# Optimization experiments

Hardware: AMD Instinct MI355X
Metric: run time of the kernel (lower is better)

Reference implementation:

```python
import jax, jax.numpy as jnp
import numpy as np

N_KNOTS = 16
DEGREE = 3
EPS = 1e-8


def make_knots(n_knots, degree):
    knots = np.zeros(n_knots, dtype=np.float32)
    for i in range(n_knots):
        if i <= degree:
            knots[i] = 0.0
        elif i >= n_knots - degree - 1:
            knots[i] = 1.0
        else:
            knots[i] = (i - degree) / (n_knots - 2 * degree - 1)
    return knots


def setup_inputs() -> dict:
    key = jax.random.key(0)
    k1, k2 = jax.random.split(key)
    x = jax.random.uniform(k1, (65536, 64), dtype=jnp.float32)
    control_points = jax.random.normal(k2, (64, 12, 64), dtype=jnp.float32)
    return {"x": x, "control_points": control_points}


def bspline_basis(x, knots_np, degree):
    # x: [B, D] in [0,1]; returns basis: [B, D, n_control_points]
    n_knots = knots_np.shape[0]
    n_intervals = n_knots - 1
    knots = jnp.asarray(knots_np)
    xe = x[..., None]  # [B, D, 1]
    left = knots[:-1]
    right = knots[1:]
    in_interval = (xe >= left) & (xe < right)
    last = (xe >= left[-1]) & (xe <= right[-1])  # include right endpoint of last interval
    basis = jnp.concatenate([in_interval[..., :-1], last], axis=-1).astype(x.dtype)
    for k in range(1, degree + 1):
        nb = n_intervals - k
        j = np.arange(nb)
        dL = knots_np[j + k] - knots_np[j]          # constants
        dR = knots_np[j + k + 1] - knots_np[j + 1]
        okL = np.abs(dL) > EPS
        okR = np.abs(dR) > EPS
        invL = jnp.asarray(np.where(okL, 1.0 / np.where(okL, dL, 1.0), 0.0).astype(np.float32))
        invR = jnp.asarray(np.where(okR, 1.0 / np.where(okR, dR, 1.0), 0.0).astype(np.float32))
        cL = (xe - knots[j]) * invL                 # [B, D, nb], zero where degenerate
        cR = (knots[j + k + 1] - xe) * invR
        basis = cL * basis[..., :nb] + cR * basis[..., 1:nb + 1]
    return basis


def reference(x, control_points):
    # x: [B, in_dim]; control_points: [in_dim, n_cp, out_dim]
    knots_np = make_knots(N_KNOTS, DEGREE)
    xc = jnp.clip(x, 0.0, 1.0)
    basis = bspline_basis(xc, knots_np, DEGREE)     # [B, in_dim, n_cp]
    return jnp.einsum('bic,ico->bo', basis, control_points)
```

## Files before the change

kernel.cpp:

```cpp
#include <hip/hip_runtime.h>


typedef short short8 __attribute__((ext_vector_type(8)));
typedef float f32x4 __attribute__((ext_vector_type(4)));
typedef unsigned u32x4 __attribute__((ext_vector_type(4)));

#define THREADS 256

static __device__ __forceinline__ unsigned bf16rne(float f) {
  unsigned u = __float_as_uint(f);
  return (u + 0x7FFFu + ((u >> 16) & 1u)) >> 16;
}

__global__ __launch_bounds__(256) void prep_wfrag(const float* __restrict__ cp,
                                                  unsigned* __restrict__ wfrag) {
  int id = blockIdx.x * 256 + threadIdx.x;
  int d  = id & 3;
  int l  = (id >> 2) & 63;
  int id2 = id >> 8;
  int nt = id2 / 24;
  int s  = id2 - nt * 24;
  int g  = l >> 4;
  int o  = nt * 16 + (l & 15);
  int k0 = 192 * g + 8 * s + 2 * d;
  unsigned lo = bf16rne(cp[k0 * 64 + o]);
  unsigned hi = bf16rne(cp[(k0 + 1) * 64 + o]);
  wfrag[id] = lo | (hi << 16);
}

struct Pack6 { unsigned w0, w1, w2, w3, w4, w5; };

static __device__ __forceinline__ Pack6 eval_pack(float xi) {
  xi = fminf(fmaxf(xi, 0.0f), 1.0f);
  float t9 = xi * 9.0f;
  int jj = (int)t9;
  float validf = (jj <= 8) ? 1.0f : 0.0f;
  jj = (jj > 8) ? 8 : jj;
  float fj = (float)jj;
  float u  = t9 - fj;
  float omu = 1.0f - u;
  float c1  = fminf(fj, 1.0f);
  float c2  = fminf(fj, 2.0f);
  float rdj = 9.0f - fj;
  float d2p = fminf(rdj, 2.0f);
  float d3p = fminf(rdj, 3.0f);
  float invA = (jj == 0) ? 1.0f : 0.5f;
  float invB = (jj == 8) ? 1.0f : 0.5f;
  float invC = (jj == 0) ? 1.0f : ((jj == 1) ? 0.5f : (1.0f / 3.0f));
  float invD = (jj == 0 || jj == 8) ? 0.5f : (1.0f / 3.0f);
  float invE = (jj >= 7) ? ((jj == 8) ? 1.0f : 0.5f) : (1.0f / 3.0f);
  float xkm1 = u + c1, xkm2 = u + c2;
  float k2x = d2p - u, k3x = d3p - u;
  float t0 = omu * invA;
  float A0 = omu * t0;
  float s1 = xkm1 * t0;
  float t1 = u * invB;
  float A1 = fmaf(k2x, t1, s1);
  float A2 = u * t1;
  float u0 = A0 * invC;
  float B0 = omu * u0;
  float s2 = xkm2 * u0;
  float u1 = A1 * invD;
  float B1 = fmaf(k2x, u1, s2);
  float s3 = xkm1 * u1;
  float u2 = A2 * invE;
  float B2 = fmaf(k3x, u2, s3);
  float B3 = u * u2;
  B0 *= validf; B1 *= validf; B2 *= validf; B3 *= validf;

  unsigned b0 = bf16rne(B0), b1 = bf16rne(B1), b2 = bf16rne(B2), b3 = bf16rne(B3);
  unsigned p01 = b0 | (b1 << 16);
  unsigned p23 = b2 | (b3 << 16);
  unsigned O0 = p01 << 16;
  unsigned O1 = (p01 >> 16) | (p23 << 16);
  unsigned O2 = p23 >> 16;
  int e2 = jj >> 1;
  bool odd = (jj & 1) != 0;
#define VE(q) ((q == e2) ? p01 : ((q == e2 + 1) ? p23 : 0u))
#define VO(q) ((q == e2) ? O0 : ((q == e2 + 1) ? O1 : ((q == e2 + 2) ? O2 : 0u)))
  Pack6 r;
  r.w0 = odd ? VO(0) : VE(0);
  r.w1 = odd ? VO(1) : VE(1);
  r.w2 = odd ? VO(2) : VE(2);
  r.w3 = odd ? VO(3) : VE(3);
  r.w4 = odd ? VO(4) : VE(4);
  r.w5 = odd ? VO(5) : VE(5);
#undef VE
#undef VO
  return r;
}

__global__ __launch_bounds__(THREADS, 4) void kan_mfma(const float* __restrict__ x,
                                                       const unsigned* __restrict__ wfrag,
                                                       float* __restrict__ out) {
  const int tid  = threadIdx.x;
  const int lane = tid & 63;
  const int w    = tid >> 6;
  const int m = lane & 15, g = lane >> 4;
  const long row0 = (long)blockIdx.x * 64 + (w >> 1) * 32;
  const int  ntb  = (w & 1) * 2;

  float xr0[16], xr1[16];
  {
    const float4* p0 = (const float4*)(x + (row0 + m) * 64 + g * 16);
    const float4* p1 = (const float4*)(x + (row0 + 16 + m) * 64 + g * 16);
    #pragma unroll
    for (int q = 0; q < 4; ++q) {
      float4 v = p0[q];
      xr0[4 * q] = v.x; xr0[4 * q + 1] = v.y; xr0[4 * q + 2] = v.z; xr0[4 * q + 3] = v.w;
    }
    #pragma unroll
    for (int q = 0; q < 4; ++q) {
      float4 v = p1[q];
      xr1[4 * q] = v.x; xr1[4 * q + 1] = v.y; xr1[4 * q + 2] = v.z; xr1[4 * q + 3] = v.w;
    }
  }

  f32x4 acc[2][2];
  #pragma unroll
  for (int mt = 0; mt < 2; ++mt)
    #pragma unroll
    for (int ntl = 0; ntl < 2; ++ntl)
      acc[mt][ntl] = f32x4{0.0f, 0.0f, 0.0f, 0.0f};

  const u32x4* wf4 = (const u32x4*)wfrag;

  #pragma unroll
  for (int q = 0; q < 8; ++q) {
    u32x4 bq0[3], bq1[3];
    #pragma unroll
    for (int sub = 0; sub < 3; ++sub) {
      bq0[sub] = wf4[((ntb + 0) * 24 + 3 * q + sub) * 64 + lane];
      bq1[sub] = wf4[((ntb + 1) * 24 + 3 * q + sub) * 64 + lane];
    }
    Pack6 aA = eval_pack(xr0[2 * q]);
    Pack6 aB = eval_pack(xr0[2 * q + 1]);
    Pack6 bA = eval_pack(xr1[2 * q]);
    Pack6 bB = eval_pack(xr1[2 * q + 1]);
    #pragma unroll
    for (int sub = 0; sub < 3; ++sub) {
      u32x4 qa, qb;
      if (sub == 0) {
        qa[0] = aA.w0; qa[1] = aA.w1; qa[2] = aA.w2; qa[3] = aA.w3;
        qb[0] = bA.w0; qb[1] = bA.w1; qb[2] = bA.w2; qb[3] = bA.w3;
      } else if (sub == 1) {
        qa[0] = aA.w4; qa[1] = aA.w5; qa[2] = aB.w0; qa[3] = aB.w1;
        qb[0] = bA.w4; qb[1] = bA.w5; qb[2] = bB.w0; qb[3] = bB.w1;
      } else {
        qa[0] = aB.w2; qa[1] = aB.w3; qa[2] = aB.w4; qa[3] = aB.w5;
        qb[0] = bB.w2; qb[1] = bB.w3; qb[2] = bB.w4; qb[3] = bB.w5;
      }
      short8 A0 = __builtin_bit_cast(short8, qa);
      short8 A1 = __builtin_bit_cast(short8, qb);
      short8 Bf0 = __builtin_bit_cast(short8, bq0[sub]);
      short8 Bf1 = __builtin_bit_cast(short8, bq1[sub]);
      acc[0][0] = __builtin_amdgcn_mfma_f32_16x16x32_bf16(A0, Bf0, acc[0][0], 0, 0, 0);
      acc[1][0] = __builtin_amdgcn_mfma_f32_16x16x32_bf16(A1, Bf0, acc[1][0], 0, 0, 0);
      acc[0][1] = __builtin_amdgcn_mfma_f32_16x16x32_bf16(A0, Bf1, acc[0][1], 0, 0, 0);
      acc[1][1] = __builtin_amdgcn_mfma_f32_16x16x32_bf16(A1, Bf1, acc[1][1], 0, 0, 0);
    }
  }

  #pragma unroll
  for (int mt = 0; mt < 2; ++mt)
    #pragma unroll
    for (int ntl = 0; ntl < 2; ++ntl)
      #pragma unroll
      for (int j = 0; j < 4; ++j)
        out[(row0 + mt * 16 + g * 4 + j) * 64 + (ntb + ntl) * 16 + m] = acc[mt][ntl][j];
}

extern "C" void kernel_launch(void* const* d_in, const int* in_sizes, int n_in,
                              void* d_out, int out_size, void* d_ws, size_t ws_size,
                              hipStream_t stream) {
  const float* x  = (const float*)d_in[0];
  const float* cp = (const float*)d_in[1];
  float* out = (float*)d_out;
  unsigned* wfrag = (unsigned*)d_ws;

  hipLaunchKernelGGL(prep_wfrag, dim3(96), dim3(256), 0, stream, cp, wfrag);
  const int rows = in_sizes[0] / 64;
  hipLaunchKernelGGL(kan_mfma, dim3(rows / 64), dim3(THREADS), 0, stream,
                     x, wfrag, out);
}
```

Before: 100.8 us.

## Give each wave 16 rows by all 64 outputs and pack basis via 64-bit shifts

Each wave now owns 16 rows and all four output tiles, instead of 32 rows and two output tiles. Each basis value is therefore evaluated once per wave rather than twice across paired waves, and the A fragments are built with a 64-bit shift of the packed bf16 quad instead of a chain of selects. The cost is that every wave loads twice as many weight fragments (4x3 u32x4 per step), which raises global/L2 traffic and register pressure.

```diff
diff --git a/kernel.cpp b/kernel.cpp
--- a/kernel.cpp
+++ b/kernel.cpp
@@ -4,6 +4,7 @@
 typedef short short8 __attribute__((ext_vector_type(8)));
 typedef float f32x4 __attribute__((ext_vector_type(4)));
 typedef unsigned u32x4 __attribute__((ext_vector_type(4)));
+typedef unsigned long long u64;
 
 #define THREADS 256
 
@@ -28,9 +29,7 @@
   wfrag[id] = lo | (hi << 16);
 }
 
-struct Pack6 { unsigned w0, w1, w2, w3, w4, w5; };
-
-static __device__ __forceinline__ Pack6 eval_pack(float xi) {
+static __device__ __forceinline__ void eval_chunks(float xi, u64& c0, u64& c1, u64& c2) {
   xi = fminf(fmaxf(xi, 0.0f), 1.0f);
   float t9 = xi * 9.0f;
   int jj = (int)t9;
@@ -39,8 +38,8 @@
   float fj = (float)jj;
   float u  = t9 - fj;
   float omu = 1.0f - u;
-  float c1  = fminf(fj, 1.0f);
-  float c2  = fminf(fj, 2.0f);
+  float k1c = fminf(fj, 1.0f);
+  float k2c = fminf(fj, 2.0f);
   float rdj = 9.0f - fj;
   float d2p = fminf(rdj, 2.0f);
   float d3p = fminf(rdj, 3.0f);
@@ -49,7 +48,7 @@
   float invC = (jj == 0) ? 1.0f : ((jj == 1) ? 0.5f : (1.0f / 3.0f));
   float invD = (jj == 0 || jj == 8) ? 0.5f : (1.0f / 3.0f);
   float invE = (jj >= 7) ? ((jj == 8) ? 1.0f : 0.5f) : (1.0f / 3.0f);
-  float xkm1 = u + c1, xkm2 = u + c2;
+  float xkm1 = u + k1c, xkm2 = u + k2c;
   float k2x = d2p - u, k3x = d3p - u;
   float t0 = omu * invA;
   float A0 = omu * t0;
@@ -68,26 +67,20 @@
   float B3 = u * u2;
   B0 *= validf; B1 *= validf; B2 *= validf; B3 *= validf;
 
-  unsigned b0 = bf16rne(B0), b1 = bf16rne(B1), b2 = bf16rne(B2), b3 = bf16rne(B3);
-  unsigned p01 = b0 | (b1 << 16);
-  unsigned p23 = b2 | (b3 << 16);
-  unsigned O0 = p01 << 16;
-  unsigned O1 = (p01 >> 16) | (p23 << 16);
-  unsigned O2 = p23 >> 16;
-  int e2 = jj >> 1;
-  bool odd = (jj & 1) != 0;
-#define VE(q) ((q == e2) ? p01 : ((q == e2 + 1) ? p23 : 0u))
-#define VO(q) ((q == e2) ? O0 : ((q == e2 + 1) ? O1 : ((q == e2 + 2) ? O2 : 0u)))
-  Pack6 r;
-  r.w0 = odd ? VO(0) : VE(0);
-  r.w1 = odd ? VO(1) : VE(1);
-  r.w2 = odd ? VO(2) : VE(2);
-  r.w3 = odd ? VO(3) : VE(3);
-  r.w4 = odd ? VO(4) : VE(4);
-  r.w5 = odd ? VO(5) : VE(5);
-#undef VE
-#undef VO
-  return r;
+  unsigned lo = bf16rne(B0) | (bf16rne(B1) << 16);
+  unsigned hi = bf16rne(B2) | (bf16rne(B3) << 16);
+  u64 P = (u64)lo | ((u64)hi << 32);
+  int s0 = jj << 4;
+  c0 = (s0 < 64) ? (P << (s0 & 63)) : 0ull;
+  c1 = (s0 < 64) ? ((s0 == 0) ? 0ull : (P >> ((64 - s0) & 63)))
+                 : ((s0 < 128) ? (P << ((s0 - 64) & 63)) : 0ull);
+  c2 = (s0 > 64) ? (P >> ((128 - s0) & 63)) : 0ull;
+}
+
+static __device__ __forceinline__ short8 mk_frag(u64 lo64, u64 hi64) {
+  u32x4 q = { (unsigned)lo64, (unsigned)(lo64 >> 32),
+              (unsigned)hi64, (unsigned)(hi64 >> 32) };
+  return __builtin_bit_cast(short8, q);
 }
 
 __global__ __launch_bounds__(THREADS, 4) void kan_mfma(const float* __restrict__ x,
@@ -97,77 +90,52 @@
   const int lane = tid & 63;
   const int w    = tid >> 6;
   const int m = lane & 15, g = lane >> 4;
-  const long row0 = (long)blockIdx.x * 64 + (w >> 1) * 32;
-  const int  ntb  = (w & 1) * 2;
+  const long row0 = (long)blockIdx.x * 64 + w * 16;
 
-  float xr0[16], xr1[16];
+  float xr[16];
   {
     const float4* p0 = (const float4*)(x + (row0 + m) * 64 + g * 16);
-    const float4* p1 = (const float4*)(x + (row0 + 16 + m) * 64 + g * 16);
     #pragma unroll
     for (int q = 0; q < 4; ++q) {
       float4 v = p0[q];
-      xr0[4 * q] = v.x; xr0[4 * q + 1] = v.y; xr0[4 * q + 2] = v.z; xr0[4 * q + 3] = v.w;
-    }
-    #pragma unroll
-    for (int q = 0; q < 4; ++q) {
-      float4 v = p1[q];
-      xr1[4 * q] = v.x; xr1[4 * q + 1] = v.y; xr1[4 * q + 2] = v.z; xr1[4 * q + 3] = v.w;
+      xr[4 * q] = v.x; xr[4 * q + 1] = v.y; xr[4 * q + 2] = v.z; xr[4 * q + 3] = v.w;
     }
   }
 
-  f32x4 acc[2][2];
+  f32x4 acc[4];
   #pragma unroll
-  for (int mt = 0; mt < 2; ++mt)
-    #pragma unroll
-    for (int ntl = 0; ntl < 2; ++ntl)
-      acc[mt][ntl] = f32x4{0.0f, 0.0f, 0.0f, 0.0f};
+  for (int nt = 0; nt < 4; ++nt) acc[nt] = f32x4{0.0f, 0.0f, 0.0f, 0.0f};
 
   const u32x4* wf4 = (const u32x4*)wfrag;
 
   #pragma unroll
   for (int q = 0; q < 8; ++q) {
-    u32x4 bq0[3], bq1[3];
+    u32x4 bq[4][3];
     #pragma unroll
-    for (int sub = 0; sub < 3; ++sub) {
-      bq0[sub] = wf4[((ntb + 0) * 24 + 3 * q + sub) * 64 + lane];
-      bq1[sub] = wf4[((ntb + 1) * 24 + 3 * q + sub) * 64 + lane];
-    }
-    Pack6 aA = eval_pack(xr0[2 * q]);
-    Pack6 aB = eval_pack(xr0[2 * q + 1]);
-    Pack6 bA = eval_pack(xr1[2 * q]);
-    Pack6 bB = eval_pack(xr1[2 * q + 1]);
+    for (int nt = 0; nt < 4; ++nt)
+      #pragma unroll
+      for (int sub = 0; sub < 3; ++sub)
+        bq[nt][sub] = wf4[(nt * 24 + 3 * q + sub) * 64 + lane];
+
+    u64 a0, a1, a2, b0, b1, b2;
+    eval_chunks(xr[2 * q],     a0, a1, a2);
+    eval_chunks(xr[2 * q + 1], b0, b1, b2);
+
+    short8 A[3] = { mk_frag(a0, a1), mk_frag(a2, b0), mk_frag(b1, b2) };
+
     #pragma unroll
-    for (int sub = 0; sub < 3; ++sub) {
-      u32x4 qa, qb;
-      if (sub == 0) {
-        qa[0] = aA.w0; qa[1] = aA.w1; qa[2] = aA.w2; qa[3] = aA.w3;
-        qb[0] = bA.w0; qb[1] = bA.w1; qb[2] = bA.w2; qb[3] = bA.w3;
-      } else if (sub == 1) {
-        qa[0] = aA.w4; qa[1] = aA.w5; qa[2] = aB.w0; qa[3] = aB.w1;
-        qb[0] = bA.w4; qb[1] = bA.w5; qb[2] = bB.w0; qb[3] = bB.w1;
-      } else {
-        qa[0] = aB.w2; qa[1] = aB.w3; qa[2] = aB.w4; qa[3] = aB.w5;
-        qb[0] = bB.w2; qb[1] = bB.w3; qb[2] = bB.w4; qb[3] = bB.w5;
-      }
-      short8 A0 = __builtin_bit_cast(short8, qa);
-      short8 A1 = __builtin_bit_cast(short8, qb);
-      short8 Bf0 = __builtin_bit_cast(short8, bq0[sub]);
-      short8 Bf1 = __builtin_bit_cast(short8, bq1[sub]);
-      acc[0][0] = __builtin_amdgcn_mfma_f32_16x16x32_bf16(A0, Bf0, acc[0][0], 0, 0, 0);
-      acc[1][0] = __builtin_amdgcn_mfma_f32_16x16x32_bf16(A1, Bf0, acc[1][0], 0, 0, 0);
-      acc[0][1] = __builtin_amdgcn_mfma_f32_16x16x32_bf16(A0, Bf1, acc[0][1], 0, 0, 0);
-      acc[1][1] = __builtin_amdgcn_mfma_f32_16x16x32_bf16(A1, Bf1, acc[1][1], 0, 0, 0);
-    }
+    for (int sub = 0; sub < 3; ++sub)
+      #pragma unroll
+      for (int nt = 0; nt < 4; ++nt)
+        acc[nt] = __builtin_amdgcn_mfma_f32_16x16x32_bf16(
+            A[sub], __builtin_bit_cast(short8, bq[nt][sub]), acc[nt], 0, 0, 0);
   }
 
   #pragma unroll
-  for (int mt = 0; mt < 2; ++mt)
+  for (int nt = 0; nt < 4; ++nt)
     #pragma unroll
-    for (int ntl = 0; ntl < 2; ++ntl)
-      #pragma unroll
-      for (int j = 0; j < 4; ++j)
-        out[(row0 + mt * 16 + g * 4 + j) * 64 + (ntb + ntl) * 16 + m] = acc[mt][ntl][j];
+    for (int j = 0; j < 4; ++j)
+      out[(row0 + g * 4 + j) * 64 + nt * 16 + m] = acc[nt][j];
 }
 
 extern "C" void kernel_launch(void* const* d_in, const int* in_sizes, int n_in,
```

Result: faster. 84.78 us (-15.9%).
